# Optimization experiments

Hardware: AMD Instinct MI355X
Metric: run time of the kernel (lower is better)

## Reference

```python
import jax, jax.numpy as jnp
import numpy as np

B, L, D_MODEL, N_HEADS = 4, 2048, 1024, 16
HEAD_DIM = D_MODEL // N_HEADS


def setup_inputs() -> dict:
    key = jax.random.key(0)
    ks = jax.random.split(key, 11)
    s = 1.0 / np.sqrt(D_MODEL)
    return {
        "queries": jax.random.normal(ks[0], (B, L, D_MODEL), jnp.float32),
        "keys": jax.random.normal(ks[1], (B, L, D_MODEL), jnp.float32),
        "values": jax.random.normal(ks[2], (B, L, D_MODEL), jnp.float32),
        "Wq": jax.random.normal(ks[3], (D_MODEL, D_MODEL), jnp.float32) * s,
        "bq": jnp.zeros((D_MODEL,), jnp.float32),
        "Wk": jax.random.normal(ks[4], (D_MODEL, D_MODEL), jnp.float32) * s,
        "bk": jnp.zeros((D_MODEL,), jnp.float32),
        "Wv": jax.random.normal(ks[5], (D_MODEL, D_MODEL), jnp.float32) * s,
        "bv": jnp.zeros((D_MODEL,), jnp.float32),
        "Wo": jax.random.normal(ks[6], (D_MODEL, D_MODEL), jnp.float32) * s,
        "bo": jnp.zeros((D_MODEL,), jnp.float32),
    }


def reference(queries, keys, values, Wq, bq, Wk, bk, Wv, bv, Wo, bo):
    Bsz, Lq, _ = queries.shape
    S = keys.shape[1]
    H, E = N_HEADS, HEAD_DIM
    # QKV projections (weights stored [in, out])
    q = (queries @ Wq + bq).reshape(Bsz, Lq, H, E)
    k = (keys @ Wk + bk).reshape(Bsz, S, H, E)
    v = (values @ Wv + bv).reshape(Bsz, S, H, E)
    scale = 1.0 / np.sqrt(E)
    # scores: [B, H, L, S]
    scores = jnp.einsum("blhe,bshe->bhls", q, k)
    A = jax.nn.softmax(scale * scores, axis=-1)
    # context: [B, L, H, E] -> [B, L, D]
    ctx = jnp.einsum("bhls,bshd->blhd", A, v).reshape(Bsz, Lq, H * E)
    out = ctx @ Wo + bo
    return out
```

## Files before the change

### kernel.cpp

```cpp
#include <hip/hip_runtime.h>

#define BATCH 4
#define SEQ   2048
#define DMODEL 1024
#define NHEADS 16
#define HDIM  64
#define MROWS (BATCH * SEQ)

typedef float f32x4 __attribute__((ext_vector_type(4)));
typedef short s16x8 __attribute__((ext_vector_type(8)));
typedef short s16x4 __attribute__((ext_vector_type(4)));
typedef unsigned short u16;

#define MFMA32K(a, b, c) __builtin_amdgcn_mfma_f32_16x16x32_bf16((a), (b), (c), 0, 0, 0)
#define MFMA16K(a, b, c) __builtin_amdgcn_mfma_f32_16x16x16bf16_1k((a), (b), (c), 0, 0, 0)

__device__ __forceinline__ u16 f2bf(float x) {
    unsigned int u = __builtin_bit_cast(unsigned int, x);
    unsigned int r = u + 0x7fffu + ((u >> 16) & 1u);
    return (u16)(r >> 16);
}

#if __has_builtin(__builtin_amdgcn_cvt_pk_bf16_f32)
__device__ __forceinline__ unsigned int pack2bf(float a, float b) {
    auto r = __builtin_amdgcn_cvt_pk_bf16_f32(a, b);
    return __builtin_bit_cast(unsigned int, r);
}
#else
__device__ __forceinline__ unsigned int pack2bf(float a, float b) {
    return (unsigned int)f2bf(a) | ((unsigned int)f2bf(b) << 16);
}
#endif

__device__ __forceinline__ void dma16(const u16* g, const u16* l) {
    __builtin_amdgcn_global_load_lds(
        (const __attribute__((address_space(1))) unsigned int*)g,
        (__attribute__((address_space(3))) unsigned int*)l, 16, 0, 0);
}

__global__ __launch_bounds__(256) void convk3(
    const float* __restrict__ s0, const float* __restrict__ s1,
    const float* __restrict__ s2, u16* __restrict__ d0, u16* __restrict__ d1,
    u16* __restrict__ d2) {
    const int z = blockIdx.y;
    const float* src = (z == 0) ? s0 : (z == 1) ? s1 : s2;
    u16* dst = (z == 0) ? d0 : (z == 1) ? d1 : d2;
    const int i = blockIdx.x * 256 + threadIdx.x;
    float4 a = ((const float4*)src)[i * 2];
    float4 b = ((const float4*)src)[i * 2 + 1];
    uint4 o;
    o.x = pack2bf(a.x, a.y); o.y = pack2bf(a.z, a.w);
    o.z = pack2bf(b.x, b.y); o.w = pack2bf(b.z, b.w);
    *(uint4*)(dst + (size_t)i * 8) = o;
}

__global__ __launch_bounds__(256) void wconv(const float* __restrict__ W0,
                                             const float* __restrict__ W1,
                                             const float* __restrict__ W2,
                                             const float* __restrict__ W3,
                                             u16* __restrict__ Wt) {
    __shared__ u16 tile[64][80];
    const int t = threadIdx.x;
    const int mtx = blockIdx.z;
    const float* W = (mtx == 0) ? W0 : (mtx == 1) ? W1 : (mtx == 2) ? W2 : W3;
    u16* out = Wt + (size_t)mtx * DMODEL * DMODEL;
    const int n0 = blockIdx.x * 64, k0 = blockIdx.y * 64;
#pragma unroll
    for (int j = 0; j < 4; ++j) {
        int k = j * 16 + (t >> 4);
        int c = (t & 15) * 4;
        float4 v = *(const float4*)(W + (size_t)(k0 + k) * DMODEL + n0 + c);
        tile[c + 0][k] = f2bf(v.x);
        tile[c + 1][k] = f2bf(v.y);
        tile[c + 2][k] = f2bf(v.z);
        tile[c + 3][k] = f2bf(v.w);
    }
    __syncthreads();
#pragma unroll
    for (int i2 = 0; i2 < 2; ++i2) {
        int n = i2 * 32 + (t >> 3), ck = (t & 7) * 8;
        uint4 v = *(const uint4*)(&tile[n][ck]);
        *(uint4*)(out + (size_t)(n0 + n) * DMODEL + k0 + ck) = v;
    }
}

__global__ __launch_bounds__(256) void gemm_qkv(
    const u16* __restrict__ Aq, const u16* __restrict__ Ak,
    const u16* __restrict__ Av, const u16* __restrict__ Wt,
    const float* __restrict__ biq, const float* __restrict__ bik,
    const float* __restrict__ biv, u16* __restrict__ oq, u16* __restrict__ ok,
    u16* __restrict__ ov, float sq) {
    __shared__ u16 As[128 * 32];
    __shared__ u16 Bs[128 * 32];
    const int t = threadIdx.x;
    const int w = t >> 6, lane = t & 63, quad = lane >> 4, l16 = lane & 15;
    const int z = blockIdx.z;
    const u16* A = (z == 0) ? Aq : (z == 1) ? Ak : Av;
    const u16* B = Wt + (size_t)z * DMODEL * DMODEL;
    const float* bias = (z == 0) ? biq : (z == 1) ? bik : biv;
    u16* C = (z == 0) ? oq : (z == 1) ? ok : ov;
    const float scale = (z == 0) ? sq : 1.0f;
    const int m0 = blockIdx.x * 128, n0 = blockIdx.y * 128;
    const int wm = (w >> 1) * 64, wn = (w & 1) * 64;
    const int lr = lane >> 2, lc = (lane & 3) * 8;

    f32x4 acc[4][4] = {};

    for (int k0 = 0; k0 < DMODEL; k0 += 32) {
#pragma unroll
        for (int j = 0; j < 2; ++j) {
            int row = w * 32 + j * 16;
            dma16(A + (size_t)(m0 + row + lr) * DMODEL + k0 + lc, &As[row * 32]);
            dma16(B + (size_t)(n0 + row + lr) * DMODEL + k0 + lc, &Bs[row * 32]);
        }
        __syncthreads();
        s16x8 af[4], bf[4];
#pragma unroll
        for (int mt = 0; mt < 4; ++mt)
            af[mt] = *(const s16x8*)(&As[(wm + mt * 16 + l16) * 32 + quad * 8]);
#pragma unroll
        for (int nt = 0; nt < 4; ++nt)
            bf[nt] = *(const s16x8*)(&Bs[(wn + nt * 16 + l16) * 32 + quad * 8]);
#pragma unroll
        for (int mt = 0; mt < 4; ++mt)
#pragma unroll
            for (int nt = 0; nt < 4; ++nt)
                acc[mt][nt] = MFMA32K(af[mt], bf[nt], acc[mt][nt]);
        __syncthreads();
    }

#pragma unroll
    for (int mt = 0; mt < 4; ++mt)
#pragma unroll
        for (int nt = 0; nt < 4; ++nt) {
            int col = n0 + wn + nt * 16 + l16;
            float bv_ = bias[col];
#pragma unroll
            for (int r = 0; r < 4; ++r) {
                int row = m0 + wm + mt * 16 + quad * 4 + r;
                C[(size_t)row * DMODEL + col] = f2bf((acc[mt][nt][r] + bv_) * scale);
            }
        }
}

__global__ __launch_bounds__(256) void gemm_o(const u16* __restrict__ A,
                                              const u16* __restrict__ Bt,
                                              const float* __restrict__ bias,
                                              float* __restrict__ Cp) {
    __shared__ u16 As[128 * 32];
    __shared__ u16 Bs[128 * 32];
    const int t = threadIdx.x;
    const int w = t >> 6, lane = t & 63, quad = lane >> 4, l16 = lane & 15;
    const int m0 = blockIdx.x * 128, n0 = blockIdx.y * 128;
    const int wm = (w >> 1) * 64, wn = (w & 1) * 64;
    const int lr = lane >> 2, lc = (lane & 3) * 8;

    f32x4 acc[4][4] = {};

    for (int k0 = 0; k0 < DMODEL; k0 += 32) {
#pragma unroll
        for (int j = 0; j < 2; ++j) {
            int row = w * 32 + j * 16;
            dma16(A + (size_t)(m0 + row + lr) * DMODEL + k0 + lc, &As[row * 32]);
            dma16(Bt + (size_t)(n0 + row + lr) * DMODEL + k0 + lc, &Bs[row * 32]);
        }
        __syncthreads();
        s16x8 af[4], bf[4];
#pragma unroll
        for (int mt = 0; mt < 4; ++mt)
            af[mt] = *(const s16x8*)(&As[(wm + mt * 16 + l16) * 32 + quad * 8]);
#pragma unroll
        for (int nt = 0; nt < 4; ++nt)
            bf[nt] = *(const s16x8*)(&Bs[(wn + nt * 16 + l16) * 32 + quad * 8]);
#pragma unroll
        for (int mt = 0; mt < 4; ++mt)
#pragma unroll
            for (int nt = 0; nt < 4; ++nt)
                acc[mt][nt] = MFMA32K(af[mt], bf[nt], acc[mt][nt]);
        __syncthreads();
    }

#pragma unroll
    for (int mt = 0; mt < 4; ++mt)
#pragma unroll
        for (int nt = 0; nt < 4; ++nt) {
            int col = n0 + wn + nt * 16 + l16;
            float bv_ = bias[col];
#pragma unroll
            for (int r = 0; r < 4; ++r) {
                int row = m0 + wm + mt * 16 + quad * 4 + r;
                Cp[(size_t)row * DMODEL + col] = acc[mt][nt][r] + bv_;
            }
        }
}

__global__ __launch_bounds__(256) void attn3(const u16* __restrict__ qb,
                                             const u16* __restrict__ kb,
                                             const u16* __restrict__ vb,
                                             u16* __restrict__ ctxb) {
    __shared__ u16 Ks[64 * 64];
    __shared__ u16 Vt[64 * 72];
    const int t = threadIdx.x;
    const int w = t >> 6, lane = t & 63, quad = lane >> 4, l16 = lane & 15;
    const int h = blockIdx.x, b = blockIdx.z, q0 = blockIdx.y * 128;

    s16x8 bq[2][2];
#pragma unroll
    for (int qs = 0; qs < 2; ++qs) {
        size_t base = (size_t)(b * SEQ + q0 + w * 32 + qs * 16 + l16) * DMODEL + h * HDIM + quad * 8;
        bq[qs][0] = *(const s16x8*)(qb + base);
        bq[qs][1] = *(const s16x8*)(qb + base + 32);
    }

    const int krow = lane >> 3;
    const int kunit = (lane & 7) ^ (krow & 7);

    float lsum[2] = {0.0f, 0.0f};
    f32x4 o[2][4] = {};

    for (int s0 = 0; s0 < SEQ; s0 += 64) {
        __syncthreads();
#pragma unroll
        for (int j = 0; j < 2; ++j) {
            int row = w * 16 + j * 8 + krow;
            dma16(kb + (size_t)(b * SEQ + s0 + row) * DMODEL + h * HDIM + kunit * 8,
                  &Ks[(w * 16 + j * 8) * 64]);
        }
#pragma unroll
        for (int i = 0; i < 2; ++i) {
            int idx = i * 256 + t;
            int key = idx >> 3, seg = idx & 7;
            union { uint4 v; u16 s[8]; } u;
            u.v = *(const uint4*)(vb + (size_t)(b * SEQ + s0 + key) * DMODEL + h * HDIM + seg * 8);
            int col = (((key >> 3) ^ seg) << 3) + (key & 7);
#pragma unroll
            for (int ii = 0; ii < 8; ++ii)
                Vt[(seg * 8 + ii) * 72 + col] = u.s[ii];
        }
        __syncthreads();

        s16x8 ak[4][2];
#pragma unroll
        for (int kt = 0; kt < 4; ++kt) {
            int row = kt * 16 + l16;
#pragma unroll
            for (int hf = 0; hf < 2; ++hf) {
                int un = (hf * 4 + quad) ^ (l16 & 7);
                ak[kt][hf] = *(const s16x8*)(&Ks[row * 64 + un * 8]);
            }
        }

        unsigned int pk[2][4][2];
#pragma unroll
        for (int qs = 0; qs < 2; ++qs) {
            f32x4 sc[4];
#pragma unroll
            for (int kt = 0; kt < 4; ++kt) {
                f32x4 zz = {0.0f, 0.0f, 0.0f, 0.0f};
                zz = MFMA32K(ak[kt][0], bq[qs][0], zz);
                sc[kt] = MFMA32K(ak[kt][1], bq[qs][1], zz);
            }
            float rs = 0.0f;
            float p[4][4];
#pragma unroll
            for (int kt = 0; kt < 4; ++kt)
#pragma unroll
                for (int r = 0; r < 4; ++r) {
                    p[kt][r] = __builtin_amdgcn_exp2f(sc[kt][r]);
                    rs += p[kt][r];
                }
            rs += __shfl_xor(rs, 16);
            rs += __shfl_xor(rs, 32);
            lsum[qs] += rs;
#pragma unroll
            for (int kt = 0; kt < 4; ++kt) {
                pk[qs][kt][0] = pack2bf(p[kt][0], p[kt][1]);
                pk[qs][kt][1] = pack2bf(p[kt][2], p[kt][3]);
            }
        }

#pragma unroll
        for (int mt = 0; mt < 4; ++mt) {
            const int dim = mt * 16 + l16;
            const int swz = (dim >> 3) & 7;
            const int rowoff = dim * 72;
#pragma unroll
            for (int kt = 0; kt < 4; ++kt) {
                int col = ((((kt * 2) + (quad >> 1)) ^ swz) << 3) + ((quad & 1) << 2);
                s16x4 av = *(const s16x4*)(&Vt[rowoff + col]);
#pragma unroll
                for (int qs = 0; qs < 2; ++qs) {
                    union { unsigned int u[2]; s16x4 v; } pb;
                    pb.u[0] = pk[qs][kt][0];
                    pb.u[1] = pk[qs][kt][1];
                    o[qs][mt] = MFMA16K(av, pb.v, o[qs][mt]);
                }
            }
        }
    }

#pragma unroll
    for (int qs = 0; qs < 2; ++qs) {
        float rl = 1.0f / lsum[qs];
        size_t rowbase = (size_t)(b * SEQ + q0 + w * 32 + qs * 16 + l16) * DMODEL + h * HDIM;
#pragma unroll
        for (int mt = 0; mt < 4; ++mt)
#pragma unroll
            for (int rr = 0; rr < 2; ++rr) {
                unsigned int v = pack2bf(o[qs][mt][rr * 2] * rl, o[qs][mt][rr * 2 + 1] * rl);
                *(unsigned int*)(&ctxb[rowbase + mt * 16 + quad * 4 + rr * 2]) = v;
            }
    }
}

extern "C" void kernel_launch(void* const* d_in, const int* in_sizes, int n_in,
                              void* d_out, int out_size, void* d_ws, size_t ws_size,
                              hipStream_t stream) {
    const float* queries = (const float*)d_in[0];
    const float* keys    = (const float*)d_in[1];
    const float* values  = (const float*)d_in[2];
    const float* Wq = (const float*)d_in[3];
    const float* bq = (const float*)d_in[4];
    const float* Wk = (const float*)d_in[5];
    const float* bk = (const float*)d_in[6];
    const float* Wv = (const float*)d_in[7];
    const float* bv = (const float*)d_in[8];
    const float* Wo = (const float*)d_in[9];
    const float* bo = (const float*)d_in[10];
    float* out = (float*)d_out;

    char* ws = (char*)d_ws;
    u16* Wt   = (u16*)ws;
    u16* aq   = (u16*)(ws + ((size_t)8 << 20));
    u16* ak   = (u16*)(ws + ((size_t)24 << 20));
    u16* av   = (u16*)(ws + ((size_t)40 << 20));
    u16* qbuf = (u16*)(ws + ((size_t)56 << 20));
    u16* kbuf = (u16*)(ws + ((size_t)72 << 20));
    u16* vbuf = (u16*)(ws + ((size_t)88 << 20));
    u16* ctxb = qbuf;

    const size_t WSZ = (size_t)DMODEL * DMODEL;
    const float S2 = 0.125f * 1.44269504088896340736f;

    dim3 blk(256);

    wconv<<<dim3(16, 16, 4), blk, 0, stream>>>(Wq, Wk, Wv, Wo, Wt);
    convk3<<<dim3(4096, 3), blk, 0, stream>>>(queries, keys, values, aq, ak, av);

    gemm_qkv<<<dim3(64, 8, 3), blk, 0, stream>>>(aq, ak, av, Wt,
                                                 bq, bk, bv, qbuf, kbuf, vbuf, S2);

    attn3<<<dim3(NHEADS, SEQ / 128, BATCH), blk, 0, stream>>>(qbuf, kbuf, vbuf, ctxb);

    gemm_o<<<dim3(64, 8), blk, 0, stream>>>(ctxb, Wt + 3 * WSZ, bo, out);
}
```

Before: 377.5 us.

## Double-buffer attention K/V tiles, widen GEMM K-step with swizzled LDS

```diff
diff --git a/kernel.cpp b/kernel.cpp
--- a/kernel.cpp
+++ b/kernel.cpp
@@ -29,6 +29,22 @@
 #else
 __device__ __forceinline__ unsigned int pack2bf(float a, float b) {
     return (unsigned int)f2bf(a) | ((unsigned int)f2bf(b) << 16);
+}
+#endif
+
+#if __has_builtin(__builtin_amdgcn_perm)
+__device__ __forceinline__ unsigned int perm_lo16(unsigned int y, unsigned int x) {
+    return __builtin_amdgcn_perm(y, x, 0x05040100u);
+}
+__device__ __forceinline__ unsigned int perm_hi16(unsigned int y, unsigned int x) {
+    return __builtin_amdgcn_perm(y, x, 0x07060302u);
+}
+#else
+__device__ __forceinline__ unsigned int perm_lo16(unsigned int y, unsigned int x) {
+    return (x & 0xffffu) | (y << 16);
+}
+__device__ __forceinline__ unsigned int perm_hi16(unsigned int y, unsigned int x) {
+    return (x >> 16) | (y & 0xffff0000u);
 }
 #endif
 
@@ -90,8 +106,8 @@
     const float* __restrict__ biq, const float* __restrict__ bik,
     const float* __restrict__ biv, u16* __restrict__ oq, u16* __restrict__ ok,
     u16* __restrict__ ov, float sq) {
-    __shared__ u16 As[128 * 32];
-    __shared__ u16 Bs[128 * 32];
+    __shared__ u16 As[128 * 64];
+    __shared__ u16 Bs[128 * 64];
     const int t = threadIdx.x;
     const int w = t >> 6, lane = t & 63, quad = lane >> 4, l16 = lane & 15;
     const int z = blockIdx.z;
@@ -102,30 +118,40 @@
     const float scale = (z == 0) ? sq : 1.0f;
     const int m0 = blockIdx.x * 128, n0 = blockIdx.y * 128;
     const int wm = (w >> 1) * 64, wn = (w & 1) * 64;
-    const int lr = lane >> 2, lc = (lane & 3) * 8;
+    const int lr = lane >> 3;
+    const int gu = (lane & 7) ^ lr;
 
     f32x4 acc[4][4] = {};
 
-    for (int k0 = 0; k0 < DMODEL; k0 += 32) {
-#pragma unroll
-        for (int j = 0; j < 2; ++j) {
-            int row = w * 32 + j * 16;
-            dma16(A + (size_t)(m0 + row + lr) * DMODEL + k0 + lc, &As[row * 32]);
-            dma16(B + (size_t)(n0 + row + lr) * DMODEL + k0 + lc, &Bs[row * 32]);
+    for (int k0 = 0; k0 < DMODEL; k0 += 64) {
+#pragma unroll
+        for (int j = 0; j < 4; ++j) {
+            int row = w * 32 + j * 8;
+            dma16(A + (size_t)(m0 + row + lr) * DMODEL + k0 + gu * 8, &As[row * 64]);
+            dma16(B + (size_t)(n0 + row + lr) * DMODEL + k0 + gu * 8, &Bs[row * 64]);
         }
         __syncthreads();
-        s16x8 af[4], bf[4];
-#pragma unroll
-        for (int mt = 0; mt < 4; ++mt)
-            af[mt] = *(const s16x8*)(&As[(wm + mt * 16 + l16) * 32 + quad * 8]);
-#pragma unroll
-        for (int nt = 0; nt < 4; ++nt)
-            bf[nt] = *(const s16x8*)(&Bs[(wn + nt * 16 + l16) * 32 + quad * 8]);
-#pragma unroll
-        for (int mt = 0; mt < 4; ++mt)
-#pragma unroll
-            for (int nt = 0; nt < 4; ++nt)
-                acc[mt][nt] = MFMA32K(af[mt], bf[nt], acc[mt][nt]);
+#pragma unroll
+        for (int kh = 0; kh < 2; ++kh) {
+            s16x8 af[4], bf[4];
+#pragma unroll
+            for (int mt = 0; mt < 4; ++mt) {
+                int row = wm + mt * 16 + l16;
+                int un = (kh * 4 + quad) ^ (l16 & 7);
+                af[mt] = *(const s16x8*)(&As[row * 64 + un * 8]);
+            }
+#pragma unroll
+            for (int nt = 0; nt < 4; ++nt) {
+                int row = wn + nt * 16 + l16;
+                int un = (kh * 4 + quad) ^ (l16 & 7);
+                bf[nt] = *(const s16x8*)(&Bs[row * 64 + un * 8]);
+            }
+#pragma unroll
+            for (int mt = 0; mt < 4; ++mt)
+#pragma unroll
+                for (int nt = 0; nt < 4; ++nt)
+                    acc[mt][nt] = MFMA32K(af[mt], bf[nt], acc[mt][nt]);
+        }
         __syncthreads();
     }
 
@@ -147,36 +173,46 @@
                                               const u16* __restrict__ Bt,
                                               const float* __restrict__ bias,
                                               float* __restrict__ Cp) {
-    __shared__ u16 As[128 * 32];
-    __shared__ u16 Bs[128 * 32];
+    __shared__ u16 As[128 * 64];
+    __shared__ u16 Bs[128 * 64];
     const int t = threadIdx.x;
     const int w = t >> 6, lane = t & 63, quad = lane >> 4, l16 = lane & 15;
     const int m0 = blockIdx.x * 128, n0 = blockIdx.y * 128;
     const int wm = (w >> 1) * 64, wn = (w & 1) * 64;
-    const int lr = lane >> 2, lc = (lane & 3) * 8;
+    const int lr = lane >> 3;
+    const int gu = (lane & 7) ^ lr;
 
     f32x4 acc[4][4] = {};
 
-    for (int k0 = 0; k0 < DMODEL; k0 += 32) {
-#pragma unroll
-        for (int j = 0; j < 2; ++j) {
-            int row = w * 32 + j * 16;
-            dma16(A + (size_t)(m0 + row + lr) * DMODEL + k0 + lc, &As[row * 32]);
-            dma16(Bt + (size_t)(n0 + row + lr) * DMODEL + k0 + lc, &Bs[row * 32]);
+    for (int k0 = 0; k0 < DMODEL; k0 += 64) {
+#pragma unroll
+        for (int j = 0; j < 4; ++j) {
+            int row = w * 32 + j * 8;
+            dma16(A + (size_t)(m0 + row + lr) * DMODEL + k0 + gu * 8, &As[row * 64]);
+            dma16(Bt + (size_t)(n0 + row + lr) * DMODEL + k0 + gu * 8, &Bs[row * 64]);
         }
         __syncthreads();
-        s16x8 af[4], bf[4];
-#pragma unroll
-        for (int mt = 0; mt < 4; ++mt)
-            af[mt] = *(const s16x8*)(&As[(wm + mt * 16 + l16) * 32 + quad * 8]);
-#pragma unroll
-        for (int nt = 0; nt < 4; ++nt)
-            bf[nt] = *(const s16x8*)(&Bs[(wn + nt * 16 + l16) * 32 + quad * 8]);
-#pragma unroll
-        for (int mt = 0; mt < 4; ++mt)
-#pragma unroll
-            for (int nt = 0; nt < 4; ++nt)
-                acc[mt][nt] = MFMA32K(af[mt], bf[nt], acc[mt][nt]);
+#pragma unroll
+        for (int kh = 0; kh < 2; ++kh) {
+            s16x8 af[4], bf[4];
+#pragma unroll
+            for (int mt = 0; mt < 4; ++mt) {
+                int row = wm + mt * 16 + l16;
+                int un = (kh * 4 + quad) ^ (l16 & 7);
+                af[mt] = *(const s16x8*)(&As[row * 64 + un * 8]);
+            }
+#pragma unroll
+            for (int nt = 0; nt < 4; ++nt) {
+                int row = wn + nt * 16 + l16;
+                int un = (kh * 4 + quad) ^ (l16 & 7);
+                bf[nt] = *(const s16x8*)(&Bs[row * 64 + un * 8]);
+            }
+#pragma unroll
+            for (int mt = 0; mt < 4; ++mt)
+#pragma unroll
+                for (int nt = 0; nt < 4; ++nt)
+                    acc[mt][nt] = MFMA32K(af[mt], bf[nt], acc[mt][nt]);
+        }
         __syncthreads();
     }
 
@@ -194,12 +230,12 @@
         }
 }
 
-__global__ __launch_bounds__(256) void attn3(const u16* __restrict__ qb,
+__global__ __launch_bounds__(256) void attn4(const u16* __restrict__ qb,
                                              const u16* __restrict__ kb,
                                              const u16* __restrict__ vb,
                                              u16* __restrict__ ctxb) {
-    __shared__ u16 Ks[64 * 64];
-    __shared__ u16 Vt[64 * 72];
+    __shared__ u16 Ks[2][64 * 64];
+    __shared__ u16 Vt[2][64 * 72];
     const int t = threadIdx.x;
     const int w = t >> 6, lane = t & 63, quad = lane >> 4, l16 = lane & 15;
     const int h = blockIdx.x, b = blockIdx.z, q0 = blockIdx.y * 128;
@@ -214,68 +250,84 @@
 
     const int krow = lane >> 3;
     const int kunit = (lane & 7) ^ (krow & 7);
-
-    float lsum[2] = {0.0f, 0.0f};
+    const int kp = t >> 3;
+    const int seg = t & 7;
+    const int colp = (((kp >> 2) ^ seg) << 3) + ((kp & 3) * 2);
+
+    const size_t kbase = (size_t)(b * SEQ) * DMODEL + h * HDIM;
+
+    const s16x4 vone = {(short)0x3F80, (short)0x3F80, (short)0x3F80, (short)0x3F80};
+
+    f32x4 lacc[2] = {};
     f32x4 o[2][4] = {};
 
-    for (int s0 = 0; s0 < SEQ; s0 += 64) {
-        __syncthreads();
-#pragma unroll
-        for (int j = 0; j < 2; ++j) {
-            int row = w * 16 + j * 8 + krow;
-            dma16(kb + (size_t)(b * SEQ + s0 + row) * DMODEL + h * HDIM + kunit * 8,
-                  &Ks[(w * 16 + j * 8) * 64]);
-        }
-#pragma unroll
-        for (int i = 0; i < 2; ++i) {
-            int idx = i * 256 + t;
-            int key = idx >> 3, seg = idx & 7;
-            union { uint4 v; u16 s[8]; } u;
-            u.v = *(const uint4*)(vb + (size_t)(b * SEQ + s0 + key) * DMODEL + h * HDIM + seg * 8);
-            int col = (((key >> 3) ^ seg) << 3) + (key & 7);
-#pragma unroll
-            for (int ii = 0; ii < 8; ++ii)
-                Vt[(seg * 8 + ii) * 72 + col] = u.s[ii];
-        }
-        __syncthreads();
-
-        s16x8 ak[4][2];
+#pragma unroll
+    for (int j = 0; j < 2; ++j) {
+        int row = w * 16 + j * 8 + krow;
+        dma16(kb + kbase + (size_t)row * DMODEL + kunit * 8, &Ks[0][(w * 16 + j * 8) * 64]);
+    }
+    {
+        const u16* src = vb + kbase + (size_t)(2 * kp) * DMODEL + seg * 8;
+        uint4 va = *(const uint4*)src;
+        uint4 vb2 = *(const uint4*)(src + DMODEL);
+        const unsigned int* wa = (const unsigned int*)&va;
+        const unsigned int* wb = (const unsigned int*)&vb2;
+#pragma unroll
+        for (int j = 0; j < 4; ++j) {
+            *(unsigned int*)(&Vt[0][(seg * 8 + 2 * j) * 72 + colp]) = perm_lo16(wb[j], wa[j]);
+            *(unsigned int*)(&Vt[0][(seg * 8 + 2 * j + 1) * 72 + colp]) = perm_hi16(wb[j], wa[j]);
+        }
+    }
+    __syncthreads();
+
+    for (int s = 0; s < SEQ / 64; ++s) {
+        const int cur = s & 1, nxt = cur ^ 1;
+        const bool pf = (s + 1 < SEQ / 64);
+        uint4 va, vb2;
+        if (pf) {
+            const size_t nb = kbase + (size_t)((s + 1) * 64) * DMODEL;
+#pragma unroll
+            for (int j = 0; j < 2; ++j) {
+                int row = w * 16 + j * 8 + krow;
+                dma16(kb + nb + (size_t)row * DMODEL + kunit * 8,
+                      &Ks[nxt][(w * 16 + j * 8) * 64]);
+            }
+            const u16* src = vb + nb + (size_t)(2 * kp) * DMODEL + seg * 8;
+            va = *(const uint4*)src;
+            vb2 = *(const uint4*)(src + DMODEL);
+        }
+
+        f32x4 sc[2][4];
 #pragma unroll
         for (int kt = 0; kt < 4; ++kt) {
             int row = kt * 16 + l16;
-#pragma unroll
-            for (int hf = 0; hf < 2; ++hf) {
-                int un = (hf * 4 + quad) ^ (l16 & 7);
-                ak[kt][hf] = *(const s16x8*)(&Ks[row * 64 + un * 8]);
+            int un0 = quad ^ (l16 & 7);
+            int un1 = (4 + quad) ^ (l16 & 7);
+            s16x8 ak0 = *(const s16x8*)(&Ks[cur][row * 64 + un0 * 8]);
+            s16x8 ak1 = *(const s16x8*)(&Ks[cur][row * 64 + un1 * 8]);
+#pragma unroll
+            for (int qs = 0; qs < 2; ++qs) {
+                f32x4 zz = {0.0f, 0.0f, 0.0f, 0.0f};
+                zz = MFMA32K(ak0, bq[qs][0], zz);
+                sc[qs][kt] = MFMA32K(ak1, bq[qs][1], zz);
             }
         }
 
         unsigned int pk[2][4][2];
 #pragma unroll
         for (int qs = 0; qs < 2; ++qs) {
-            f32x4 sc[4];
 #pragma unroll
             for (int kt = 0; kt < 4; ++kt) {
-                f32x4 zz = {0.0f, 0.0f, 0.0f, 0.0f};
-                zz = MFMA32K(ak[kt][0], bq[qs][0], zz);
-                sc[kt] = MFMA32K(ak[kt][1], bq[qs][1], zz);
-            }
-            float rs = 0.0f;
-            float p[4][4];
-#pragma unroll
-            for (int kt = 0; kt < 4; ++kt)
-#pragma unroll
-                for (int r = 0; r < 4; ++r) {
-                    p[kt][r] = __builtin_amdgcn_exp2f(sc[kt][r]);
-                    rs += p[kt][r];
-                }
-            rs += __shfl_xor(rs, 16);
-            rs += __shfl_xor(rs, 32);
-            lsum[qs] += rs;
-#pragma unroll
-            for (int kt = 0; kt < 4; ++kt) {
-                pk[qs][kt][0] = pack2bf(p[kt][0], p[kt][1]);
-                pk[qs][kt][1] = pack2bf(p[kt][2], p[kt][3]);
+                float p0 = __builtin_amdgcn_exp2f(sc[qs][kt][0]);
+                float p1 = __builtin_amdgcn_exp2f(sc[qs][kt][1]);
+                float p2 = __builtin_amdgcn_exp2f(sc[qs][kt][2]);
+                float p3 = __builtin_amdgcn_exp2f(sc[qs][kt][3]);
+                pk[qs][kt][0] = pack2bf(p0, p1);
+                pk[qs][kt][1] = pack2bf(p2, p3);
+                union { unsigned int u[2]; s16x4 v; } pb;
+                pb.u[0] = pk[qs][kt][0];
+                pb.u[1] = pk[qs][kt][1];
+                lacc[qs] = MFMA16K(vone, pb.v, lacc[qs]);
             }
         }
 
@@ -287,7 +339,7 @@
 #pragma unroll
             for (int kt = 0; kt < 4; ++kt) {
                 int col = ((((kt * 2) + (quad >> 1)) ^ swz) << 3) + ((quad & 1) << 2);
-                s16x4 av = *(const s16x4*)(&Vt[rowoff + col]);
+                s16x4 av = *(const s16x4*)(&Vt[cur][rowoff + col]);
 #pragma unroll
                 for (int qs = 0; qs < 2; ++qs) {
                     union { unsigned int u[2]; s16x4 v; } pb;
@@ -297,11 +349,22 @@
                 }
             }
         }
+
+        if (pf) {
+            const unsigned int* wa = (const unsigned int*)&va;
+            const unsigned int* wb = (const unsigned int*)&vb2;
+#pragma unroll
+            for (int j = 0; j < 4; ++j) {
+                *(unsigned int*)(&Vt[nxt][(seg * 8 + 2 * j) * 72 + colp]) = perm_lo16(wb[j], wa[j]);
+                *(unsigned int*)(&Vt[nxt][(seg * 8 + 2 * j + 1) * 72 + colp]) = perm_hi16(wb[j], wa[j]);
+            }
+        }
+        __syncthreads();
     }
 
 #pragma unroll
     for (int qs = 0; qs < 2; ++qs) {
-        float rl = 1.0f / lsum[qs];
+        float rl = 1.0f / lacc[qs][0];
         size_t rowbase = (size_t)(b * SEQ + q0 + w * 32 + qs * 16 + l16) * DMODEL + h * HDIM;
 #pragma unroll
         for (int mt = 0; mt < 4; ++mt)
@@ -350,7 +413,7 @@
     gemm_qkv<<<dim3(64, 8, 3), blk, 0, stream>>>(aq, ak, av, Wt,
                                                  bq, bk, bv, qbuf, kbuf, vbuf, S2);
 
-    attn3<<<dim3(NHEADS, SEQ / 128, BATCH), blk, 0, stream>>>(qbuf, kbuf, vbuf, ctxb);
+    attn4<<<dim3(NHEADS, SEQ / 128, BATCH), blk, 0, stream>>>(qbuf, kbuf, vbuf, ctxb);
 
     gemm_o<<<dim3(64, 8), blk, 0, stream>>>(ctxb, Wt + 3 * WSZ, bo, out);
 }
```

New measurement: 380.7 us. About the same (+0.9%).
